# Kernel optimization log

Measured on AMD Instinct MI355X. Metric: run time of the kernel, lower is better.

Reference implementation:

```python
import jax, jax.numpy as jnp
import numpy as np

B, S, E, H = 4, 2048, 1024, 16
D = E // H  # d_k = 64
NEG = -1000000000.0  # matches torch masked_fill constant


def setup_inputs() -> dict:
    rk = jax.random.key(0)
    kq, kk, kv, km = jax.random.split(rk, 4)
    query = jax.random.normal(kq, (B, S, E), dtype=jnp.float32)
    key = jax.random.normal(kk, (B, S, E), dtype=jnp.float32)
    value = jax.random.normal(kv, (B, S, E), dtype=jnp.float32)
    mask = jax.random.randint(km, (B, S, S), 0, 2, dtype=jnp.int32)
    return {"query": query, "key": key, "value": value, "mask": mask}


def _split_heads(x):
    # (B, S, E) -> (B, H, S, D)
    return x.reshape(B, S, H, D).transpose(0, 2, 1, 3)


def reference(query, key, value, mask):
    q = _split_heads(query)
    k = _split_heads(key)
    v = _split_heads(value)
    scale = np.float32(1.0 / np.sqrt(D))
    scores = jnp.einsum('bhqd,bhkd->bhqk', q, k) * scale  # (B,H,S,S)
    scores = jnp.where(mask[:, None, :, :] == 0, jnp.float32(NEG), scores)
    weights = jax.nn.softmax(scores, axis=-1)
    attn = jnp.einsum('bhqk,bhkd->bhqd', weights, v)  # (B,H,S,D)
    concat = attn.transpose(0, 2, 1, 3).reshape(B, S, E)
    return concat
```

## Files before the change

### kernel.cpp

```cpp
#include <hip/hip_runtime.h>
#include <hip/hip_bf16.h>
#include <math.h>

constexpr int B = 4, S = 2048, E = 1024, H = 16, D = 64;
constexpr float NEGF = -1000000000.0f;
constexpr float KSCALE = 0.125f * 1.44269504f;

typedef __attribute__((ext_vector_type(8))) short short8;
typedef __attribute__((ext_vector_type(16))) float f32x16;

__device__ inline unsigned pk2(float a, float b) {
    unsigned ua = __builtin_bit_cast(unsigned, a) + 0x8000u;
    unsigned ub = __builtin_bit_cast(unsigned, b) + 0x8000u;
    return __builtin_amdgcn_perm(ub, ua, 0x07060302u);
}
__device__ inline void gl_lds16(const void* g, void* l) {
    __builtin_amdgcn_global_load_lds(
        (const __attribute__((address_space(1))) unsigned int*)g,
        (__attribute__((address_space(3))) unsigned int*)l, 16, 0, 0);
}
__device__ inline void plswap(unsigned& a, unsigned& b) {
    asm volatile("v_permlane32_swap_b32 %0, %1" : "+v"(a), "+v"(b));
}

constexpr size_t WS_K  = 0;
constexpr size_t WS_VT = 18874368;
constexpr size_t WS_MB = 37748736;
constexpr size_t WS_NEED = 54525952;

__global__ void prep_all(const float* __restrict__ K, const float* __restrict__ V,
                         const int* __restrict__ M, char* __restrict__ ws) {
    __shared__ float Vf[64][69];
    const int bid = blockIdx.x, tid = threadIdx.x;

    {
        int g = bid * 256 + tid;
        int rowd = g >> 2, qtr = g & 3;
        int b = rowd >> 15, h = (rowd >> 11) & 15, s = rowd & 2047;
        const float* p = K + ((size_t)(b * S + s)) * E + h * 64 + qtr * 16;
        float4 v0 = *(const float4*)(p + 0),  v1 = *(const float4*)(p + 4);
        float4 v2 = *(const float4*)(p + 8),  v3 = *(const float4*)(p + 12);
        uint4 o0, o1;
        o0.x = pk2(v0.x * KSCALE, v0.y * KSCALE); o0.y = pk2(v0.z * KSCALE, v0.w * KSCALE);
        o0.z = pk2(v1.x * KSCALE, v1.y * KSCALE); o0.w = pk2(v1.z * KSCALE, v1.w * KSCALE);
        o1.x = pk2(v2.x * KSCALE, v2.y * KSCALE); o1.y = pk2(v2.z * KSCALE, v2.w * KSCALE);
        o1.z = pk2(v3.x * KSCALE, v3.y * KSCALE); o1.w = pk2(v3.z * KSCALE, v3.w * KSCALE);
        char* d = ws + WS_K + (size_t)rowd * 144 + qtr * 32;
        *(uint4*)d = o0; *(uint4*)(d + 16) = o1;
        if (qtr == 3) {
            uint4 z; z.x = z.y = z.z = z.w = 0;
            *(uint4*)(d + 32) = z;
        }
    }

    {
        int bh = bid >> 5, kt = bid & 31;
        int b = bh >> 4, h = bh & 15;
        {
            int r = tid >> 2, c4 = (tid & 3) * 16;
            const float* p = V + ((size_t)(b * S + kt * 64 + r)) * E + h * 64 + c4;
            float4 a = *(const float4*)(p + 0), bb = *(const float4*)(p + 4);
            float4 c = *(const float4*)(p + 8), dd = *(const float4*)(p + 12);
            *(float4*)&Vf[r][c4 + 0] = a;  *(float4*)&Vf[r][c4 + 4] = bb;
            *(float4*)&Vf[r][c4 + 8] = c;  *(float4*)&Vf[r][c4 + 12] = dd;
        }
        __syncthreads();
        int d = tid >> 2, sq = (tid & 3) * 16;
        float v[16];
#pragma unroll
        for (int i = 0; i < 16; ++i) v[i] = Vf[sq + i][d];
        uint4 o0, o1;
        o0.x = pk2(v[0], v[1]);   o0.y = pk2(v[2], v[3]);
        o0.z = pk2(v[4], v[5]);   o0.w = pk2(v[6], v[7]);
        o1.x = pk2(v[8], v[9]);   o1.y = pk2(v[10], v[11]);
        o1.z = pk2(v[12], v[13]); o1.w = pk2(v[14], v[15]);
        char* o = ws + WS_VT + ((size_t)(bh * 32 + kt)) * 9216 + d * 144 + sq * 2;
        *(uint4*)o = o0; *(uint4*)(o + 16) = o1;
        if (sq == 48) {
            uint4 z; z.x = z.y = z.z = z.w = 0;
            *(uint4*)(o + 32) = z;
        }
    }

    {
        unsigned* Mb = (unsigned*)(ws + WS_MB);
        const int t = bid * 256 + tid;
#pragma unroll
        for (int it = 0; it < 8; ++it) {
            int gidx = it * 524288 + t;
            int4 mv = *((const int4*)M + gidx);
            unsigned d = (mv.x ? 0xFFu : 0u) | (mv.y ? 0xFF00u : 0u)
                       | (mv.z ? 0xFF0000u : 0u) | (mv.w ? 0xFF000000u : 0u);
            int row = gidx >> 4, g = gidx & 15;
            Mb[row * 16 + (g & 1) * 8 + (g >> 1)] = d;
        }
    }
}

__global__ __launch_bounds__(256, 2)
void fa_mfma(const float* __restrict__ Q, const char* __restrict__ ws,
             float* __restrict__ O) {
    __shared__ char smem[34816];
    const int tid = threadIdx.x;
    const int w = tid >> 6, lane = tid & 63;
    const int L5 = lane & 31, h6 = lane >> 5;
    const int h = blockIdx.x & 15, b = (blockIdx.x >> 4) & 3, qt = blockIdx.x >> 6;
    const int bh = b * 16 + h;
    const int q0w = qt * 256 + w * 64;

    const char* Kws  = ws + WS_K;
    const char* Vtws = ws + WS_VT;
    const int qA = q0w + L5, qB = qA + 32;
    const char* mrowA = ws + WS_MB + ((size_t)(b * S + qA)) * 2048 + h6 * 32;
    const char* mrowB = ws + WS_MB + ((size_t)(b * S + qB)) * 2048 + h6 * 32;

    short8 qf[2][4];
#pragma unroll
    for (int nb = 0; nb < 2; ++nb)
#pragma unroll
        for (int ks = 0; ks < 4; ++ks) {
            const float* qp = Q + ((size_t)(b * S + q0w + nb * 32 + L5)) * E
                                + h * 64 + ks * 16 + h6 * 8;
            float4 a = *(const float4*)qp;
            float4 c = *(const float4*)(qp + 4);
            uint4 u;
            u.x = pk2(a.x, a.y); u.y = pk2(a.z, a.w);
            u.z = pk2(c.x, c.y); u.w = pk2(c.z, c.w);
            qf[nb][ks] = *(short8*)&u;
        }

    f32x16 acc[2][2];
#pragma unroll
    for (int mb = 0; mb < 2; ++mb)
#pragma unroll
        for (int nb = 0; nb < 2; ++nb) acc[mb][nb] = (f32x16)0.0f;
    float l0 = 0.0f, l1 = 0.0f;

    for (int ti = 0; ti < 32; ++ti) {
        const uint4 mAl = *(const uint4*)(mrowA + ti * 64);
        const uint4 mAh = *(const uint4*)(mrowA + ti * 64 + 16);
        const uint4 mBl = *(const uint4*)(mrowB + ti * 64);
        const uint4 mBh = *(const uint4*)(mrowB + ti * 64 + 16);
        const unsigned mdwA[8] = {mAl.x, mAl.y, mAl.z, mAl.w, mAh.x, mAh.y, mAh.z, mAh.w};
        const unsigned mdwB[8] = {mBl.x, mBl.y, mBl.z, mBl.w, mBh.x, mBh.y, mBh.z, mBh.w};

        __syncthreads();
        {
            const char* ksrc = Kws + ((size_t)bh * S + ti * 64) * 144;
            const char* vsrc = Vtws + ((size_t)(bh * 32 + ti)) * 9216;
#pragma unroll
            for (int c = 0; c < 5; ++c) {
                int idx = c * 4 + w;
                if (idx < 18) {
                    int off = idx * 1024;
                    const char* g = (off < 9216) ? (ksrc + off) : (vsrc + off - 9216);
                    gl_lds16(g + lane * 16, smem + off);
                }
            }
        }
        __syncthreads();

        const char* bufK = smem;
        const char* bufV = smem + 9216;

#pragma unroll
        for (int mbK = 0; mbK < 2; ++mbK) {
            short8 kf[4];
#pragma unroll
            for (int ks = 0; ks < 4; ++ks)
                kf[ks] = *(const short8*)(bufK + (mbK * 32 + L5) * 144 + ks * 32 + h6 * 16);
            short8 pf[2][2];
#pragma unroll
            for (int nb = 0; nb < 2; ++nb) {
                f32x16 s = (f32x16)0.0f;
                __builtin_amdgcn_s_setprio(1);
#pragma unroll
                for (int ks = 0; ks < 4; ++ks)
                    s = __builtin_amdgcn_mfma_f32_32x32x16_bf16(kf[ks], qf[nb][ks], s, 0, 0, 0);
                __builtin_amdgcn_s_setprio(0);

                const unsigned* mdw = nb ? mdwB : mdwA;
                float lacc = 0.0f;
                unsigned pd[8];
#pragma unroll
                for (int i = 0; i < 8; ++i) {
                    float e0 = __builtin_amdgcn_exp2f(s[2 * i]);
                    float e1 = __builtin_amdgcn_exp2f(s[2 * i + 1]);
                    unsigned pm = pk2(e0, e1);
                    const unsigned mv = mdw[mbK * 4 + (i >> 1)];
                    const unsigned am = __builtin_amdgcn_perm(
                        mv, mv, (i & 1) ? 0x03030202u : 0x01010000u);
                    pm &= am;
                    pd[i] = pm;
                    float lo = __builtin_bit_cast(float, pm << 16);
                    float hi = __builtin_bit_cast(float, pm & 0xFFFF0000u);
                    lacc += lo + hi;
                }
                if (nb) l1 += lacc; else l0 += lacc;

                plswap(pd[0], pd[2]); plswap(pd[1], pd[3]);
                plswap(pd[4], pd[6]); plswap(pd[5], pd[7]);
                uint4 f0; f0.x = pd[0]; f0.y = pd[1]; f0.z = pd[2]; f0.w = pd[3];
                uint4 f1; f1.x = pd[4]; f1.y = pd[5]; f1.z = pd[6]; f1.w = pd[7];
                pf[nb][0] = *(short8*)&f0;
                pf[nb][1] = *(short8*)&f1;
            }

#pragma unroll
            for (int mbV = 0; mbV < 2; ++mbV) {
                short8 vf[2];
#pragma unroll
                for (int s2 = 0; s2 < 2; ++s2)
                    vf[s2] = *(const short8*)(bufV + (mbV * 32 + L5) * 144
                                              + (mbK * 2 + s2) * 32 + h6 * 16);
                __builtin_amdgcn_s_setprio(1);
#pragma unroll
                for (int nb = 0; nb < 2; ++nb)
#pragma unroll
                    for (int s2 = 0; s2 < 2; ++s2)
                        acc[mbV][nb] = __builtin_amdgcn_mfma_f32_32x32x16_bf16(
                            vf[s2], pf[nb][s2], acc[mbV][nb], 0, 0, 0);
                __builtin_amdgcn_s_setprio(0);
            }
        }
    }

    char* const Pse = smem + w * 8704;
    l0 += __shfl_xor(l0, 32, 64);
    l1 += __shfl_xor(l1, 32, 64);
    const float inv[2] = {1.0f / l0, 1.0f / l1};
    __syncthreads();
#pragma unroll
    for (int nb = 0; nb < 2; ++nb) {
#pragma unroll
        for (int mb = 0; mb < 2; ++mb)
#pragma unroll
            for (int g4 = 0; g4 < 4; ++g4) {
                float4 t;
                t.x = acc[mb][nb][g4 * 4 + 0] * inv[nb];
                t.y = acc[mb][nb][g4 * 4 + 1] * inv[nb];
                t.z = acc[mb][nb][g4 * 4 + 2] * inv[nb];
                t.w = acc[mb][nb][g4 * 4 + 3] * inv[nb];
                *(float4*)(Pse + (L5 * 68 + mb * 32 + g4 * 8 + h6 * 4) * 4) = t;
            }
        __builtin_amdgcn_s_waitcnt(0xc07f);
        const int r16 = lane >> 4, dc = lane & 15;
#pragma unroll
        for (int i = 0; i < 8; ++i) {
            const int row = i * 4 + r16;
            float4 t = *(const float4*)(Pse + (row * 68 + dc * 4) * 4);
            *(float4*)(O + ((size_t)b * S + q0w + nb * 32 + row) * E + h * 64 + dc * 4) = t;
        }
        __builtin_amdgcn_s_waitcnt(0xc07f);
    }
}

constexpr int QT = 64, KT = 64, LD = D + 4;
constexpr float SCALE = 0.125f;
__global__ __launch_bounds__(256, 3)
void fa_fp32(const float* __restrict__ Q, const float* __restrict__ K,
             const float* __restrict__ V, const int* __restrict__ M,
             float* __restrict__ Out)
{
    __shared__ float Qs[QT][LD];
    __shared__ float Vs[KT][LD];
    __shared__ float KPs[KT][LD];
    const int tid = threadIdx.x, tx = tid & 15, ty = tid >> 4;
    const int bid = blockIdx.x;
    const int h = bid % H, b = (bid / H) % B, qt = bid / (H * B);
    const int q0 = qt * QT;
    {
        const int col = tx * 4;
#pragma unroll
        for (int i = 0; i < 4; ++i) {
            const int row = ty + i * 16;
            *(float4*)&Qs[row][col] = *(const float4*)&Q[((size_t)(b * S + q0 + row)) * E + h * D + col];
        }
    }
    const int qr0 = ty * 4, d0 = tx * 4;
    float acc[4][4] = {};
    float m_i[4], l_i[4];
#pragma unroll
    for (int j = 0; j < 4; ++j) { m_i[j] = -INFINITY; l_i[j] = 0.0f; }
    for (int kt = 0; kt < S; kt += KT) {
        __syncthreads();
        {
            const int col = tx * 4;
#pragma unroll
            for (int i = 0; i < 4; ++i) {
                const int row = ty + i * 16;
                const size_t g = ((size_t)(b * S + kt + row)) * E + h * D + col;
                *(float4*)&KPs[row][col] = *(const float4*)&K[g];
                *(float4*)&Vs[row][col] = *(const float4*)&V[g];
            }
        }
        __syncthreads();
        float s[4][4] = {};
#pragma unroll
        for (int d = 0; d < D; d += 4) {
            float4 a[4], bb[4];
#pragma unroll
            for (int j = 0; j < 4; ++j) a[j] = *(const float4*)&Qs[qr0 + j][d];
#pragma unroll
            for (int i = 0; i < 4; ++i) bb[i] = *(const float4*)&KPs[tx + 16 * i][d];
#pragma unroll
            for (int j = 0; j < 4; ++j)
#pragma unroll
                for (int i = 0; i < 4; ++i)
                    s[j][i] += a[j].x * bb[i].x + a[j].y * bb[i].y + a[j].z * bb[i].z + a[j].w * bb[i].w;
        }
#pragma unroll
        for (int j = 0; j < 4; ++j) {
            const int* mrow = &M[((size_t)b * S + (q0 + qr0 + j)) * S + kt];
#pragma unroll
            for (int i = 0; i < 4; ++i) {
                const int mk = mrow[tx + 16 * i];
                s[j][i] = mk ? s[j][i] * SCALE : NEGF;
            }
        }
#pragma unroll
        for (int j = 0; j < 4; ++j) {
            float tm = fmaxf(fmaxf(s[j][0], s[j][1]), fmaxf(s[j][2], s[j][3]));
#pragma unroll
            for (int off = 8; off; off >>= 1) tm = fmaxf(tm, __shfl_xor(tm, off, 16));
            const float nm = fmaxf(m_i[j], tm);
            const float alpha = __expf(m_i[j] - nm);
            m_i[j] = nm;
            float rs = 0.0f;
#pragma unroll
            for (int i = 0; i < 4; ++i) { const float p = __expf(s[j][i] - nm); s[j][i] = p; rs += p; }
#pragma unroll
            for (int off = 8; off; off >>= 1) rs += __shfl_xor(rs, off, 16);
            l_i[j] = l_i[j] * alpha + rs;
#pragma unroll
            for (int dd = 0; dd < 4; ++dd) acc[j][dd] *= alpha;
        }
        __syncthreads();
#pragma unroll
        for (int j = 0; j < 4; ++j)
#pragma unroll
            for (int i = 0; i < 4; ++i) KPs[qr0 + j][tx + 16 * i] = s[j][i];
        __syncthreads();
#pragma unroll 4
        for (int kk = 0; kk < KT; kk += 4) {
            float4 p[4], vv[4];
#pragma unroll
            for (int j = 0; j < 4; ++j) p[j] = *(const float4*)&KPs[qr0 + j][kk];
#pragma unroll
            for (int u = 0; u < 4; ++u) vv[u] = *(const float4*)&Vs[kk + u][d0];
#pragma unroll
            for (int j = 0; j < 4; ++j) {
                acc[j][0] += p[j].x * vv[0].x + p[j].y * vv[1].x + p[j].z * vv[2].x + p[j].w * vv[3].x;
                acc[j][1] += p[j].x * vv[0].y + p[j].y * vv[1].y + p[j].z * vv[2].y + p[j].w * vv[3].y;
                acc[j][2] += p[j].x * vv[0].z + p[j].y * vv[1].z + p[j].z * vv[2].z + p[j].w * vv[3].z;
                acc[j][3] += p[j].x * vv[0].w + p[j].y * vv[1].w + p[j].z * vv[2].w + p[j].w * vv[3].w;
            }
        }
    }
#pragma unroll
    for (int j = 0; j < 4; ++j) {
        const float iv = 1.0f / l_i[j];
        float4 r;
        r.x = acc[j][0] * iv; r.y = acc[j][1] * iv; r.z = acc[j][2] * iv; r.w = acc[j][3] * iv;
        *(float4*)&Out[((size_t)(b * S + q0 + qr0 + j)) * E + h * D + d0] = r;
    }
}

extern "C" void kernel_launch(void* const* d_in, const int* in_sizes, int n_in,
                              void* d_out, int out_size, void* d_ws, size_t ws_size,
                              hipStream_t stream) {
    (void)in_sizes; (void)n_in; (void)out_size;
    const float* q = (const float*)d_in[0];
    const float* k = (const float*)d_in[1];
    const float* v = (const float*)d_in[2];
    const int*   m = (const int*)d_in[3];
    float* out = (float*)d_out;

    if (ws_size >= WS_NEED) {
        char* ws = (char*)d_ws;
        prep_all<<<2048, 256, 0, stream>>>(k, v, m, ws);
        fa_mfma<<<512, 256, 0, stream>>>(q, ws, out);
    } else {
        fa_fp32<<<B * H * (S / QT), 256, 0, stream>>>(q, k, v, m, out);
    }
}
```

Measured before the change: 289.1 us.

## Shrink attention blocks to two waves of 32 queries each

Work per block drops from 4 waves × 64 queries to 2 waves × 32 queries, so each wave computes one 32-query score tile instead of two. Launch size goes from 512 to 2048 blocks of 128 threads, and shared memory shrinks to 18 KB. The intent is more concurrent blocks per CU, better latency hiding and fewer registers per thread. In exchange, each K/V tile staged into shared memory serves 4x fewer queries, so global-to-LDS traffic and K/V fragment reads per query rise.

```diff
diff --git a/kernel.cpp b/kernel.cpp
--- a/kernel.cpp
+++ b/kernel.cpp
@@ -97,65 +97,53 @@
     }
 }
 
-__global__ __launch_bounds__(256, 2)
+__global__ __launch_bounds__(128, 4)
 void fa_mfma(const float* __restrict__ Q, const char* __restrict__ ws,
              float* __restrict__ O) {
-    __shared__ char smem[34816];
+    __shared__ char smem[18432];
     const int tid = threadIdx.x;
     const int w = tid >> 6, lane = tid & 63;
     const int L5 = lane & 31, h6 = lane >> 5;
     const int h = blockIdx.x & 15, b = (blockIdx.x >> 4) & 3, qt = blockIdx.x >> 6;
     const int bh = b * 16 + h;
-    const int q0w = qt * 256 + w * 64;
+    const int q0w = qt * 64 + w * 32;
 
     const char* Kws  = ws + WS_K;
     const char* Vtws = ws + WS_VT;
-    const int qA = q0w + L5, qB = qA + 32;
+    const int qA = q0w + L5;
     const char* mrowA = ws + WS_MB + ((size_t)(b * S + qA)) * 2048 + h6 * 32;
-    const char* mrowB = ws + WS_MB + ((size_t)(b * S + qB)) * 2048 + h6 * 32;
-
-    short8 qf[2][4];
-#pragma unroll
-    for (int nb = 0; nb < 2; ++nb)
-#pragma unroll
-        for (int ks = 0; ks < 4; ++ks) {
-            const float* qp = Q + ((size_t)(b * S + q0w + nb * 32 + L5)) * E
-                                + h * 64 + ks * 16 + h6 * 8;
-            float4 a = *(const float4*)qp;
-            float4 c = *(const float4*)(qp + 4);
-            uint4 u;
-            u.x = pk2(a.x, a.y); u.y = pk2(a.z, a.w);
-            u.z = pk2(c.x, c.y); u.w = pk2(c.z, c.w);
-            qf[nb][ks] = *(short8*)&u;
-        }
-
-    f32x16 acc[2][2];
-#pragma unroll
-    for (int mb = 0; mb < 2; ++mb)
-#pragma unroll
-        for (int nb = 0; nb < 2; ++nb) acc[mb][nb] = (f32x16)0.0f;
-    float l0 = 0.0f, l1 = 0.0f;
+
+    short8 qf[4];
+#pragma unroll
+    for (int ks = 0; ks < 4; ++ks) {
+        const float* qp = Q + ((size_t)(b * S + qA)) * E + h * 64 + ks * 16 + h6 * 8;
+        float4 a = *(const float4*)qp;
+        float4 c = *(const float4*)(qp + 4);
+        uint4 u;
+        u.x = pk2(a.x, a.y); u.y = pk2(a.z, a.w);
+        u.z = pk2(c.x, c.y); u.w = pk2(c.z, c.w);
+        qf[ks] = *(short8*)&u;
+    }
+
+    f32x16 acc[2];
+#pragma unroll
+    for (int mb = 0; mb < 2; ++mb) acc[mb] = (f32x16)0.0f;
+    float l0 = 0.0f;
 
     for (int ti = 0; ti < 32; ++ti) {
         const uint4 mAl = *(const uint4*)(mrowA + ti * 64);
         const uint4 mAh = *(const uint4*)(mrowA + ti * 64 + 16);
-        const uint4 mBl = *(const uint4*)(mrowB + ti * 64);
-        const uint4 mBh = *(const uint4*)(mrowB + ti * 64 + 16);
         const unsigned mdwA[8] = {mAl.x, mAl.y, mAl.z, mAl.w, mAh.x, mAh.y, mAh.z, mAh.w};
-        const unsigned mdwB[8] = {mBl.x, mBl.y, mBl.z, mBl.w, mBh.x, mBh.y, mBh.z, mBh.w};
 
         __syncthreads();
         {
             const char* ksrc = Kws + ((size_t)bh * S + ti * 64) * 144;
             const char* vsrc = Vtws + ((size_t)(bh * 32 + ti)) * 9216;
 #pragma unroll
-            for (int c = 0; c < 5; ++c) {
-                int idx = c * 4 + w;
-                if (idx < 18) {
-                    int off = idx * 1024;
-                    const char* g = (off < 9216) ? (ksrc + off) : (vsrc + off - 9216);
-                    gl_lds16(g + lane * 16, smem + off);
-                }
+            for (int c = 0; c < 9; ++c) {
+                int off = (c * 2 + w) * 1024;
+                const char* g = (off < 9216) ? (ksrc + off) : (vsrc + off - 9216);
+                gl_lds16(g + lane * 16, smem + off);
             }
         }
         __syncthreads();
@@ -169,57 +157,48 @@
 #pragma unroll
             for (int ks = 0; ks < 4; ++ks)
                 kf[ks] = *(const short8*)(bufK + (mbK * 32 + L5) * 144 + ks * 32 + h6 * 16);
-            short8 pf[2][2];
-#pragma unroll
-            for (int nb = 0; nb < 2; ++nb) {
-                f32x16 s = (f32x16)0.0f;
+
+            f32x16 s = (f32x16)0.0f;
+            __builtin_amdgcn_s_setprio(1);
+#pragma unroll
+            for (int ks = 0; ks < 4; ++ks)
+                s = __builtin_amdgcn_mfma_f32_32x32x16_bf16(kf[ks], qf[ks], s, 0, 0, 0);
+            __builtin_amdgcn_s_setprio(0);
+
+            float lacc = 0.0f;
+            unsigned pd[8];
+#pragma unroll
+            for (int i = 0; i < 8; ++i) {
+                float e0 = __builtin_amdgcn_exp2f(s[2 * i]);
+                float e1 = __builtin_amdgcn_exp2f(s[2 * i + 1]);
+                unsigned pm = pk2(e0, e1);
+                const unsigned mv = mdwA[mbK * 4 + (i >> 1)];
+                const unsigned am = __builtin_amdgcn_perm(
+                    mv, mv, (i & 1) ? 0x03030202u : 0x01010000u);
+                pm &= am;
+                pd[i] = pm;
+                float lo = __builtin_bit_cast(float, pm << 16);
+                float hi = __builtin_bit_cast(float, pm & 0xFFFF0000u);
+                lacc += lo + hi;
+            }
+            l0 += lacc;
+
+            plswap(pd[0], pd[2]); plswap(pd[1], pd[3]);
+            plswap(pd[4], pd[6]); plswap(pd[5], pd[7]);
+            uint4 f0; f0.x = pd[0]; f0.y = pd[1]; f0.z = pd[2]; f0.w = pd[3];
+            uint4 f1; f1.x = pd[4]; f1.y = pd[5]; f1.z = pd[6]; f1.w = pd[7];
+            short8 pf0 = *(short8*)&f0;
+            short8 pf1 = *(short8*)&f1;
+
+#pragma unroll
+            for (int mbV = 0; mbV < 2; ++mbV) {
+                short8 vf0 = *(const short8*)(bufV + (mbV * 32 + L5) * 144
+                                              + (mbK * 2 + 0) * 32 + h6 * 16);
+                short8 vf1 = *(const short8*)(bufV + (mbV * 32 + L5) * 144
+                                              + (mbK * 2 + 1) * 32 + h6 * 16);
                 __builtin_amdgcn_s_setprio(1);
-#pragma unroll
-                for (int ks = 0; ks < 4; ++ks)
-                    s = __builtin_amdgcn_mfma_f32_32x32x16_bf16(kf[ks], qf[nb][ks], s, 0, 0, 0);
-                __builtin_amdgcn_s_setprio(0);
-
-                const unsigned* mdw = nb ? mdwB : mdwA;
-                float lacc = 0.0f;
-                unsigned pd[8];
-#pragma unroll
-                for (int i = 0; i < 8; ++i) {
-                    float e0 = __builtin_amdgcn_exp2f(s[2 * i]);
-                    float e1 = __builtin_amdgcn_exp2f(s[2 * i + 1]);
-                    unsigned pm = pk2(e0, e1);
-                    const unsigned mv = mdw[mbK * 4 + (i >> 1)];
-                    const unsigned am = __builtin_amdgcn_perm(
-                        mv, mv, (i & 1) ? 0x03030202u : 0x01010000u);
-                    pm &= am;
-                    pd[i] = pm;
-                    float lo = __builtin_bit_cast(float, pm << 16);
-                    float hi = __builtin_bit_cast(float, pm & 0xFFFF0000u);
-                    lacc += lo + hi;
-                }
-                if (nb) l1 += lacc; else l0 += lacc;
-
-                plswap(pd[0], pd[2]); plswap(pd[1], pd[3]);
-                plswap(pd[4], pd[6]); plswap(pd[5], pd[7]);
-                uint4 f0; f0.x = pd[0]; f0.y = pd[1]; f0.z = pd[2]; f0.w = pd[3];
-                uint4 f1; f1.x = pd[4]; f1.y = pd[5]; f1.z = pd[6]; f1.w = pd[7];
-                pf[nb][0] = *(short8*)&f0;
-                pf[nb][1] = *(short8*)&f1;
-            }
-
-#pragma unroll
-            for (int mbV = 0; mbV < 2; ++mbV) {
-                short8 vf[2];
-#pragma unroll
-                for (int s2 = 0; s2 < 2; ++s2)
-                    vf[s2] = *(const short8*)(bufV + (mbV * 32 + L5) * 144
-                                              + (mbK * 2 + s2) * 32 + h6 * 16);
-                __builtin_amdgcn_s_setprio(1);
-#pragma unroll
-                for (int nb = 0; nb < 2; ++nb)
-#pragma unroll
-                    for (int s2 = 0; s2 < 2; ++s2)
-                        acc[mbV][nb] = __builtin_amdgcn_mfma_f32_32x32x16_bf16(
-                            vf[s2], pf[nb][s2], acc[mbV][nb], 0, 0, 0);
+                acc[mbV] = __builtin_amdgcn_mfma_f32_32x32x16_bf16(vf0, pf0, acc[mbV], 0, 0, 0);
+                acc[mbV] = __builtin_amdgcn_mfma_f32_32x32x16_bf16(vf1, pf1, acc[mbV], 0, 0, 0);
                 __builtin_amdgcn_s_setprio(0);
             }
         }
@@ -227,31 +206,28 @@
 
     char* const Pse = smem + w * 8704;
     l0 += __shfl_xor(l0, 32, 64);
-    l1 += __shfl_xor(l1, 32, 64);
-    const float inv[2] = {1.0f / l0, 1.0f / l1};
+    const float inv0 = 1.0f / l0;
     __syncthreads();
 #pragma unroll
-    for (int nb = 0; nb < 2; ++nb) {
-#pragma unroll
-        for (int mb = 0; mb < 2; ++mb)
-#pragma unroll
-            for (int g4 = 0; g4 < 4; ++g4) {
-                float4 t;
-                t.x = acc[mb][nb][g4 * 4 + 0] * inv[nb];
-                t.y = acc[mb][nb][g4 * 4 + 1] * inv[nb];
-                t.z = acc[mb][nb][g4 * 4 + 2] * inv[nb];
-                t.w = acc[mb][nb][g4 * 4 + 3] * inv[nb];
-                *(float4*)(Pse + (L5 * 68 + mb * 32 + g4 * 8 + h6 * 4) * 4) = t;
-            }
-        __builtin_amdgcn_s_waitcnt(0xc07f);
+    for (int mb = 0; mb < 2; ++mb)
+#pragma unroll
+        for (int g4 = 0; g4 < 4; ++g4) {
+            float4 t;
+            t.x = acc[mb][g4 * 4 + 0] * inv0;
+            t.y = acc[mb][g4 * 4 + 1] * inv0;
+            t.z = acc[mb][g4 * 4 + 2] * inv0;
+            t.w = acc[mb][g4 * 4 + 3] * inv0;
+            *(float4*)(Pse + (L5 * 68 + mb * 32 + g4 * 8 + h6 * 4) * 4) = t;
+        }
+    __builtin_amdgcn_s_waitcnt(0xc07f);
+    {
         const int r16 = lane >> 4, dc = lane & 15;
 #pragma unroll
         for (int i = 0; i < 8; ++i) {
             const int row = i * 4 + r16;
             float4 t = *(const float4*)(Pse + (row * 68 + dc * 4) * 4);
-            *(float4*)(O + ((size_t)b * S + q0w + nb * 32 + row) * E + h * 64 + dc * 4) = t;
-        }
-        __builtin_amdgcn_s_waitcnt(0xc07f);
+            *(float4*)(O + ((size_t)b * S + q0w + row) * E + h * 64 + dc * 4) = t;
+        }
     }
 }
 
@@ -379,7 +355,7 @@
     if (ws_size >= WS_NEED) {
         char* ws = (char*)d_ws;
         prep_all<<<2048, 256, 0, stream>>>(k, v, m, ws);
-        fa_mfma<<<512, 256, 0, stream>>>(q, ws, out);
+        fa_mfma<<<2048, 128, 0, stream>>>(q, ws, out);
     } else {
         fa_fp32<<<B * H * (S / QT), 256, 0, stream>>>(q, k, v, m, out);
     }
```

Result: slower. 300.8 us (+4.0%).

## Split K and V tile loads so V load overlaps QK^T and softmax

Applied to the files above, without the earlier changes.

The combined K+V async load per tile is split in two. K is loaded first and waited on, then the V load is issued and runs while all QK^T MFMAs and the exp/mask work finish. A second wait and barrier come before the PV MFMAs. The loop is restructured so both mbK halves of P are computed and kept in registers before the PV phase. The intent is to hide V load latency behind compute, at the cost of an extra barrier and more live registers for P.

```diff
diff --git a/kernel.cpp b/kernel.cpp
--- a/kernel.cpp
+++ b/kernel.cpp
@@ -143,33 +143,44 @@
         const uint4 mBh = *(const uint4*)(mrowB + ti * 64 + 16);
         const unsigned mdwA[8] = {mAl.x, mAl.y, mAl.z, mAl.w, mAh.x, mAh.y, mAh.z, mAh.w};
         const unsigned mdwB[8] = {mBl.x, mBl.y, mBl.z, mBl.w, mBh.x, mBh.y, mBh.z, mBh.w};
-
-        __syncthreads();
-        {
-            const char* ksrc = Kws + ((size_t)bh * S + ti * 64) * 144;
-            const char* vsrc = Vtws + ((size_t)(bh * 32 + ti)) * 9216;
-#pragma unroll
-            for (int c = 0; c < 5; ++c) {
-                int idx = c * 4 + w;
-                if (idx < 18) {
-                    int off = idx * 1024;
-                    const char* g = (off < 9216) ? (ksrc + off) : (vsrc + off - 9216);
-                    gl_lds16(g + lane * 16, smem + off);
-                }
-            }
-        }
-        __syncthreads();
+        __builtin_amdgcn_sched_barrier(0);
+
+        __builtin_amdgcn_s_barrier();
+        __builtin_amdgcn_sched_barrier(0);
+
+        const char* ksrc = Kws + ((size_t)bh * S + ti * 64) * 144;
+        const char* vsrc = Vtws + ((size_t)(bh * 32 + ti)) * 9216;
+
+#pragma unroll
+        for (int c = 0; c < 5; ++c) {
+            int idx = c * 4 + w;
+            if (idx < 9)
+                gl_lds16(ksrc + idx * 1024 + lane * 16, smem + idx * 1024);
+        }
+        __builtin_amdgcn_sched_barrier(0);
+        asm volatile("s_waitcnt vmcnt(0)" ::: "memory");
+        __builtin_amdgcn_sched_barrier(0);
+        __builtin_amdgcn_s_barrier();
+        __builtin_amdgcn_sched_barrier(0);
+
+#pragma unroll
+        for (int c = 0; c < 5; ++c) {
+            int idx = c * 4 + w;
+            if (idx >= 9 && idx < 18)
+                gl_lds16(vsrc + (idx - 9) * 1024 + lane * 16, smem + idx * 1024);
+        }
+        __builtin_amdgcn_sched_barrier(0);
 
         const char* bufK = smem;
         const char* bufV = smem + 9216;
 
+        short8 pf[2][2][2];
 #pragma unroll
         for (int mbK = 0; mbK < 2; ++mbK) {
             short8 kf[4];
 #pragma unroll
             for (int ks = 0; ks < 4; ++ks)
                 kf[ks] = *(const short8*)(bufK + (mbK * 32 + L5) * 144 + ks * 32 + h6 * 16);
-            short8 pf[2][2];
 #pragma unroll
             for (int nb = 0; nb < 2; ++nb) {
                 f32x16 s = (f32x16)0.0f;
@@ -202,27 +213,35 @@
                 plswap(pd[4], pd[6]); plswap(pd[5], pd[7]);
                 uint4 f0; f0.x = pd[0]; f0.y = pd[1]; f0.z = pd[2]; f0.w = pd[3];
                 uint4 f1; f1.x = pd[4]; f1.y = pd[5]; f1.z = pd[6]; f1.w = pd[7];
-                pf[nb][0] = *(short8*)&f0;
-                pf[nb][1] = *(short8*)&f1;
-            }
-
+                pf[mbK][nb][0] = *(short8*)&f0;
+                pf[mbK][nb][1] = *(short8*)&f1;
+            }
+        }
+
+        __builtin_amdgcn_sched_barrier(0);
+        asm volatile("s_waitcnt vmcnt(0)" ::: "memory");
+        __builtin_amdgcn_sched_barrier(0);
+        __builtin_amdgcn_s_barrier();
+        __builtin_amdgcn_sched_barrier(0);
+
+#pragma unroll
+        for (int mbK = 0; mbK < 2; ++mbK)
 #pragma unroll
             for (int mbV = 0; mbV < 2; ++mbV) {
-                short8 vf[2];
-#pragma unroll
-                for (int s2 = 0; s2 < 2; ++s2)
-                    vf[s2] = *(const short8*)(bufV + (mbV * 32 + L5) * 144
-                                              + (mbK * 2 + s2) * 32 + h6 * 16);
+                short8 vf0 = *(const short8*)(bufV + (mbV * 32 + L5) * 144
+                                              + (mbK * 2 + 0) * 32 + h6 * 16);
+                short8 vf1 = *(const short8*)(bufV + (mbV * 32 + L5) * 144
+                                              + (mbK * 2 + 1) * 32 + h6 * 16);
                 __builtin_amdgcn_s_setprio(1);
 #pragma unroll
-                for (int nb = 0; nb < 2; ++nb)
-#pragma unroll
-                    for (int s2 = 0; s2 < 2; ++s2)
-                        acc[mbV][nb] = __builtin_amdgcn_mfma_f32_32x32x16_bf16(
-                            vf[s2], pf[nb][s2], acc[mbV][nb], 0, 0, 0);
+                for (int nb = 0; nb < 2; ++nb) {
+                    acc[mbV][nb] = __builtin_amdgcn_mfma_f32_32x32x16_bf16(
+                        vf0, pf[mbK][nb][0], acc[mbV][nb], 0, 0, 0);
+                    acc[mbV][nb] = __builtin_amdgcn_mfma_f32_32x32x16_bf16(
+                        vf1, pf[mbK][nb][1], acc[mbV][nb], 0, 0, 0);
+                }
                 __builtin_amdgcn_s_setprio(0);
             }
-        }
     }
 
     char* const Pse = smem + w * 8704;
```

Result: no change. 290.3 us (+0.4%).
